# Performance work log

Measured on AMD Instinct MI355X. Metric: run time of the kernel, lower is better.

The kernel has to match this reference:

```python
import jax, jax.numpy as jnp
import numpy as np

EPS = 1e-6

def setup_inputs() -> dict:
    key = jax.random.key(0)
    N, E, d_i, d_o = 2048, 65536, 128, 128
    k = jax.random.split(key, 8)
    x = jax.random.normal(k[0], (N, d_i), dtype=jnp.float32)
    src = jax.random.randint(k[1], (E,), 0, N)
    tgt = jax.random.randint(k[2], (E,), 0, N)
    adj = jnp.zeros((N, N), dtype=jnp.float32)  # unused by forward math
    # incidence matrices: Msrc[n,e]=1 iff src[e]==n, Mtgt[n,e]=1 iff tgt[e]==n
    Msrc = jax.nn.one_hot(src, N, dtype=jnp.float32).T  # [N,E]
    Mtgt = jax.nn.one_hot(tgt, N, dtype=jnp.float32).T  # [N,E]
    # xavier-uniform linear weights, stored as [in, out]
    lim_f = float(np.sqrt(6.0 / (2 * d_i + d_o)))
    lim_w = float(np.sqrt(6.0 / (2 * d_i + 1)))
    fW = jax.random.uniform(k[3], (2 * d_i, d_o), minval=-lim_f, maxval=lim_f, dtype=jnp.float32)
    fb = jax.random.normal(k[4], (d_o,), dtype=jnp.float32) * 0.01
    wW = jax.random.uniform(k[5], (2 * d_i, 1), minval=-lim_w, maxval=lim_w, dtype=jnp.float32)
    wb = jax.random.normal(k[6], (1,), dtype=jnp.float32) * 0.01
    return {"x": x, "adj": adj, "src": src, "tgt": tgt, "Msrc": Msrc,
            "Mtgt": Mtgt, "fW": fW, "fb": fb, "wW": wW, "wb": wb}

def reference(x, adj, src, tgt, Msrc, Mtgt, fW, fb, wW, wb):
    # gather endpoint features per edge and concatenate: [E, 2*d_i]
    h = jnp.concatenate([x[src], x[tgt]], axis=1)
    y = jax.nn.relu(h @ fW + fb)          # [E, d_o] edge messages
    a = h @ wW + wb                        # [E, 1] attention logits
    a_exp = jnp.exp(a - jnp.max(a, axis=0, keepdims=True))  # global-max-stabilized exp
    a_sum = Mtgt @ a_exp + EPS             # [N, 1] per-target softmax denominator
    o = (Mtgt @ (y * a_exp)) / a_sum       # [N, d_o] attention-weighted aggregation
    return o
```

## Files before the change

### kernel.cpp

```cpp
#include <hip/hip_runtime.h>
#include <math.h>

#define NN 2048
#define D  128
#define EE 65536
#define EPSF 1e-6f

__global__ void k0_init(float* __restrict__ o, float* __restrict__ a_sum,
                        unsigned int* __restrict__ amax_bits) {
    int i = blockIdx.x * blockDim.x + threadIdx.x;
    if (i < NN * D) o[i] = 0.f;
    if (i < NN) a_sum[i] = 0.f;
    if (i == 0) *amax_bits = 0xFF800000u;
}

__global__ __launch_bounds__(128) void k1_node_proj(
        const float* __restrict__ x, const float* __restrict__ fW,
        const float* __restrict__ wW,
        float* __restrict__ U, float* __restrict__ V,
        float* __restrict__ p, float* __restrict__ q) {
    int n = blockIdx.x;
    int t = threadIdx.x;
    __shared__ float xs[D];
    xs[t] = x[n * D + t];
    __syncthreads();
    float u = 0.f, v = 0.f;
#pragma unroll 8
    for (int k = 0; k < D; ++k) {
        float xv = xs[k];
        u = fmaf(xv, fW[k * D + t], u);
        v = fmaf(xv, fW[(k + D) * D + t], v);
    }
    U[n * D + t] = u;
    V[n * D + t] = v;

    float pp = xs[t] * wW[t];
    float qq = xs[t] * wW[D + t];
#pragma unroll
    for (int off = 32; off > 0; off >>= 1) {
        pp += __shfl_down(pp, off, 64);
        qq += __shfl_down(qq, off, 64);
    }
    __shared__ float red[4];
    int wave = t >> 6;
    if ((t & 63) == 0) { red[wave * 2] = pp; red[wave * 2 + 1] = qq; }
    __syncthreads();
    if (t == 0) {
        p[n] = red[0] + red[2];
        q[n] = red[1] + red[3];
    }
}

__global__ __launch_bounds__(256) void k2a_logit_max(
        const int* __restrict__ src, const int* __restrict__ tgt,
        const float* __restrict__ p, const float* __restrict__ q,
        const float* __restrict__ wb,
        float* __restrict__ a, unsigned int* __restrict__ amax_bits) {
    int i = blockIdx.x * blockDim.x + threadIdx.x;
    float local = -INFINITY;
    float wbv = wb[0];
    for (int e = i; e < EE; e += gridDim.x * blockDim.x) {
        float ae = p[src[e]] + q[tgt[e]] + wbv;
        a[e] = ae;
        local = fmaxf(local, ae);
    }
#pragma unroll
    for (int off = 32; off > 0; off >>= 1)
        local = fmaxf(local, __shfl_down(local, off, 64));
    __shared__ float smax[4];
    if ((threadIdx.x & 63) == 0) smax[threadIdx.x >> 6] = local;
    __syncthreads();
    if (threadIdx.x == 0) {
        float m = fmaxf(fmaxf(smax[0], smax[1]), fmaxf(smax[2], smax[3]));
        if (m >= 0.f) atomicMax((int*)amax_bits, __float_as_int(m));
        else          atomicMin(amax_bits, __float_as_uint(m));
    }
}

__global__ __launch_bounds__(256) void k2b_exp_sum(
        const int* __restrict__ tgt, float* __restrict__ a,
        const unsigned int* __restrict__ amax_bits,
        float* __restrict__ a_sum) {
    float amax = __uint_as_float(*amax_bits);
    int i = blockIdx.x * blockDim.x + threadIdx.x;
    for (int e = i; e < EE; e += gridDim.x * blockDim.x) {
        float ae = expf(a[e] - amax);
        a[e] = ae;
        atomicAdd(&a_sum[tgt[e]], ae);
    }
}

__global__ __launch_bounds__(256) void k3_scatter(
        const int* __restrict__ src, const int* __restrict__ tgt,
        const float* __restrict__ U, const float* __restrict__ V,
        const float* __restrict__ fb, const float* __restrict__ aexp,
        float* __restrict__ o) {
    const int total = EE * D;
    for (int idx = blockIdx.x * blockDim.x + threadIdx.x; idx < total;
         idx += gridDim.x * blockDim.x) {
        int e = idx >> 7;
        int c = idx & (D - 1);
        int s = src[e], t = tgt[e];
        float yv = U[s * D + c] + V[t * D + c] + fb[c];
        yv = fmaxf(yv, 0.f) * aexp[e];
        atomicAdd(&o[t * D + c], yv);
    }
}

__global__ __launch_bounds__(256) void k4_finalize(
        float* __restrict__ o, const float* __restrict__ a_sum) {
    int i = blockIdx.x * blockDim.x + threadIdx.x;
    if (i < NN * D) o[i] /= (a_sum[i >> 7] + EPSF);
}

extern "C" void kernel_launch(void* const* d_in, const int* in_sizes, int n_in,
                              void* d_out, int out_size, void* d_ws, size_t ws_size,
                              hipStream_t stream) {
    const float* x   = (const float*)d_in[0];
    const int*   src = (const int*)d_in[2];
    const int*   tgt = (const int*)d_in[3];
    const float* fW  = (const float*)d_in[6];
    const float* fb  = (const float*)d_in[7];
    const float* wW  = (const float*)d_in[8];
    const float* wb  = (const float*)d_in[9];
    float* o = (float*)d_out;

    float* ws = (float*)d_ws;
    float* U     = ws;
    float* V     = U + NN * D;
    float* p     = V + NN * D;
    float* q     = p + NN;
    float* a     = q + NN;
    float* a_sum = a + EE;
    unsigned int* amax_bits = (unsigned int*)(a_sum + NN);

    k0_init<<<(NN * D + 255) / 256, 256, 0, stream>>>(o, a_sum, amax_bits);
    k1_node_proj<<<NN, 128, 0, stream>>>(x, fW, wW, U, V, p, q);
    k2a_logit_max<<<EE / 256, 256, 0, stream>>>(src, tgt, p, q, wb, a, amax_bits);
    k2b_exp_sum<<<EE / 256, 256, 0, stream>>>(tgt, a, amax_bits, a_sum);
    k3_scatter<<<(EE * D) / 256, 256, 0, stream>>>(src, tgt, U, V, fb, a, o);
    k4_finalize<<<(NN * D + 255) / 256, 256, 0, stream>>>(o, a_sum);
}
```

Baseline: 873.6 us.

## Replace atomic edge scatter with CSR-by-target gather aggregation

Builds a CSR grouping of edges by target node (count, single-block scan, atomic fill), then aggregates per node with one block per target, computing exp, the denominator and the weighted sum in registers. This removes EE*D float atomics on the output plus the separate exp-sum and finalize kernels and the output zeroing. It adds a serial single-block scan and an atomic fill pass. Edge order within each row is nondeterministic, so the float summation order can vary between runs.

```diff
diff --git a/kernel.cpp b/kernel.cpp
--- a/kernel.cpp
+++ b/kernel.cpp
@@ -6,11 +6,9 @@
 #define EE 65536
 #define EPSF 1e-6f
 
-__global__ void k0_init(float* __restrict__ o, float* __restrict__ a_sum,
-                        unsigned int* __restrict__ amax_bits) {
+__global__ void k0_init(int* __restrict__ counts, unsigned int* __restrict__ amax_bits) {
     int i = blockIdx.x * blockDim.x + threadIdx.x;
-    if (i < NN * D) o[i] = 0.f;
-    if (i < NN) a_sum[i] = 0.f;
+    if (i < NN) counts[i] = 0;
     if (i == 0) *amax_bits = 0xFF800000u;
 }
 
@@ -51,18 +49,21 @@
     }
 }
 
-__global__ __launch_bounds__(256) void k2a_logit_max(
+__global__ __launch_bounds__(256) void k2_logit_max_count(
         const int* __restrict__ src, const int* __restrict__ tgt,
         const float* __restrict__ p, const float* __restrict__ q,
         const float* __restrict__ wb,
-        float* __restrict__ a, unsigned int* __restrict__ amax_bits) {
+        float* __restrict__ a, unsigned int* __restrict__ amax_bits,
+        int* __restrict__ counts) {
     int i = blockIdx.x * blockDim.x + threadIdx.x;
     float local = -INFINITY;
     float wbv = wb[0];
     for (int e = i; e < EE; e += gridDim.x * blockDim.x) {
-        float ae = p[src[e]] + q[tgt[e]] + wbv;
+        int t = tgt[e];
+        float ae = p[src[e]] + q[t] + wbv;
         a[e] = ae;
         local = fmaxf(local, ae);
+        atomicAdd(&counts[t], 1);
     }
 #pragma unroll
     for (int off = 32; off > 0; off >>= 1)
@@ -77,40 +78,66 @@
     }
 }
 
-__global__ __launch_bounds__(256) void k2b_exp_sum(
-        const int* __restrict__ tgt, float* __restrict__ a,
-        const unsigned int* __restrict__ amax_bits,
-        float* __restrict__ a_sum) {
-    float amax = __uint_as_float(*amax_bits);
-    int i = blockIdx.x * blockDim.x + threadIdx.x;
-    for (int e = i; e < EE; e += gridDim.x * blockDim.x) {
-        float ae = expf(a[e] - amax);
-        a[e] = ae;
-        atomicAdd(&a_sum[tgt[e]], ae);
+__global__ __launch_bounds__(256) void k_scan(const int* __restrict__ counts,
+                                              int* __restrict__ rowptr,
+                                              int* __restrict__ cursor) {
+    __shared__ int sums[256];
+    int t = threadIdx.x;
+    int base = t * 8;
+    int local[8];
+    int s = 0;
+#pragma unroll
+    for (int i = 0; i < 8; ++i) { local[i] = s; s += counts[base + i]; }
+    sums[t] = s;
+    __syncthreads();
+    for (int off = 1; off < 256; off <<= 1) {
+        int v = sums[t];
+        int add = (t >= off) ? sums[t - off] : 0;
+        __syncthreads();
+        sums[t] = v + add;
+        __syncthreads();
+    }
+    int prefix = (t > 0) ? sums[t - 1] : 0;
+#pragma unroll
+    for (int i = 0; i < 8; ++i) {
+        int rp = prefix + local[i];
+        rowptr[base + i] = rp;
+        cursor[base + i] = rp;
+    }
+    if (t == 255) rowptr[NN] = sums[255];
+}
+
+__global__ __launch_bounds__(256) void k_fill(const int* __restrict__ tgt,
+                                              int* __restrict__ cursor,
+                                              int* __restrict__ elist) {
+    int e = blockIdx.x * blockDim.x + threadIdx.x;
+    if (e < EE) {
+        int pos = atomicAdd(&cursor[tgt[e]], 1);
+        elist[pos] = e;
     }
 }
 
-__global__ __launch_bounds__(256) void k3_scatter(
-        const int* __restrict__ src, const int* __restrict__ tgt,
+__global__ __launch_bounds__(128) void k_agg(
+        const int* __restrict__ rowptr, const int* __restrict__ elist,
+        const int* __restrict__ src, const float* __restrict__ a,
+        const unsigned int* __restrict__ amax_bits,
         const float* __restrict__ U, const float* __restrict__ V,
-        const float* __restrict__ fb, const float* __restrict__ aexp,
-        float* __restrict__ o) {
-    const int total = EE * D;
-    for (int idx = blockIdx.x * blockDim.x + threadIdx.x; idx < total;
-         idx += gridDim.x * blockDim.x) {
-        int e = idx >> 7;
-        int c = idx & (D - 1);
-        int s = src[e], t = tgt[e];
-        float yv = U[s * D + c] + V[t * D + c] + fb[c];
-        yv = fmaxf(yv, 0.f) * aexp[e];
-        atomicAdd(&o[t * D + c], yv);
+        const float* __restrict__ fb, float* __restrict__ o) {
+    int n = blockIdx.x;
+    int c = threadIdx.x;
+    float amax = __uint_as_float(*amax_bits);
+    float vn = V[n * D + c] + fb[c];
+    float acc = 0.f, den = 0.f;
+    int jb = rowptr[n], je = rowptr[n + 1];
+    for (int j = jb; j < je; ++j) {
+        int e = elist[j];
+        float aexp = expf(a[e] - amax);
+        int s = src[e];
+        float yv = fmaxf(U[s * D + c] + vn, 0.f);
+        acc = fmaf(yv, aexp, acc);
+        den += aexp;
     }
-}
-
-__global__ __launch_bounds__(256) void k4_finalize(
-        float* __restrict__ o, const float* __restrict__ a_sum) {
-    int i = blockIdx.x * blockDim.x + threadIdx.x;
-    if (i < NN * D) o[i] /= (a_sum[i >> 7] + EPSF);
+    o[n * D + c] = acc / (den + EPSF);
 }
 
 extern "C" void kernel_launch(void* const* d_in, const int* in_sizes, int n_in,
@@ -131,13 +158,17 @@
     float* p     = V + NN * D;
     float* q     = p + NN;
     float* a     = q + NN;
-    float* a_sum = a + EE;
-    unsigned int* amax_bits = (unsigned int*)(a_sum + NN);
+    unsigned int* amax_bits = (unsigned int*)(a + EE);
+    int* counts = (int*)(amax_bits + 8);
+    int* rowptr = counts + NN;
+    int* cursor = rowptr + NN + 8;
+    int* elist  = cursor + NN;
 
-    k0_init<<<(NN * D + 255) / 256, 256, 0, stream>>>(o, a_sum, amax_bits);
+    k0_init<<<(NN + 255) / 256, 256, 0, stream>>>(counts, amax_bits);
     k1_node_proj<<<NN, 128, 0, stream>>>(x, fW, wW, U, V, p, q);
-    k2a_logit_max<<<EE / 256, 256, 0, stream>>>(src, tgt, p, q, wb, a, amax_bits);
-    k2b_exp_sum<<<EE / 256, 256, 0, stream>>>(tgt, a, amax_bits, a_sum);
-    k3_scatter<<<(EE * D) / 256, 256, 0, stream>>>(src, tgt, U, V, fb, a, o);
-    k4_finalize<<<(NN * D + 255) / 256, 256, 0, stream>>>(o, a_sum);
+    k2_logit_max_count<<<EE / 256, 256, 0, stream>>>(src, tgt, p, q, wb, a,
+                                                     amax_bits, counts);
+    k_scan<<<1, 256, 0, stream>>>(counts, rowptr, cursor);
+    k_fill<<<EE / 256, 256, 0, stream>>>(tgt, cursor, elist);
+    k_agg<<<NN, 128, 0, stream>>>(rowptr, elist, src, a, amax_bits, U, V, fb, o);
 }
```

Result: faster. 837.2 us (-4.2%).
